# Kernel tuning notes

Hardware: AMD Instinct MI355X
Metric: run time of the kernel (lower is better)

The kernel has to match this reference:

```python
import jax, jax.numpy as jnp
import numpy as np

N, H, O, E, K = 131072, 128, 128, 8, 2


def setup_inputs() -> dict:
    key = jax.random.key(0)
    k1, k2, k3, k4 = jax.random.split(key, 4)
    x = jax.random.normal(k1, (N, H), dtype=jnp.float32)
    w_gate = jax.random.normal(k2, (H, E), dtype=jnp.float32) * 0.02
    w_noise = jax.random.normal(k3, (H, E), dtype=jnp.float32) * 0.02
    w_expert = jax.random.normal(k4, (E, H, O), dtype=jnp.float32) * (1.0 / np.sqrt(H))
    b_expert = jnp.zeros((E, O), dtype=jnp.float32)
    return {"x": x, "w_gate": w_gate, "w_noise": w_noise,
            "w_expert": w_expert, "b_expert": b_expert, "top_k": K}


def _gates(x, w_gate, top_k):
    # Noisy top-k gating (eval mode: noise term w_noise is inactive).
    logits = x @ w_gate                              # [N, E]
    top_vals, top_idx = jax.lax.top_k(logits, top_k)  # [N, K]
    top_gates = jax.nn.softmax(top_vals, axis=-1)     # renormalize over top-k
    n = logits.shape[0]
    rows = jnp.arange(n)[:, None]                     # [N, 1]
    gates = jnp.zeros_like(logits).at[rows, top_idx].set(top_gates)  # [N, E] sparse
    return gates


def reference(x, w_gate, w_noise, w_expert, b_expert, top_k):
    gates = _gates(x, w_gate, top_k)                                  # [N, E]
    # Dense (mathematically identical) dispatch/combine: every expert FFN
    # applied per token, weighted by its (mostly-zero) gate.
    expert_out = jnp.einsum('nh,eho->neo', x, w_expert) + b_expert     # [N, E, O]
    out = jnp.einsum('ne,neo->no', gates, expert_out)                  # [N, O]
    return out
```

## Files before the change

kernel.cpp:

```cpp
#include <hip/hip_runtime.h>
#include <math.h>

typedef __bf16 bf16x8 __attribute__((ext_vector_type(8)));
typedef float f32x16 __attribute__((ext_vector_type(16)));

#define NTOK 131072
#define HDIM 128
#define ODIM 128
#define NEXP 8

__device__ __forceinline__ unsigned short f2bf(float f){
  union { float f; unsigned u; } v; v.f = f;
  unsigned r = v.u + 0x7FFFu + ((v.u >> 16) & 1u);
  return (unsigned short)(r >> 16);
}

__global__ void pack_w(const float* __restrict__ we, const float* __restrict__ be,
                       unsigned short* __restrict__ pw){
  int f = blockIdx.x * 256 + threadIdx.x;
  int l  = f & 63;
  int kt = (f >> 6) % 9;
  int emt = f / (64 * 9);
  int mt = emt & 3;
  int e  = emt >> 2;
  int o  = (mt << 5) + (l & 31);
  unsigned short vals[8];
#pragma unroll
  for (int j = 0; j < 8; ++j){
    int kl = ((l >> 5) << 3) + j;
    float v;
    if (kt < 8){
      int h = kt * 16 + kl;
      v = we[(e * HDIM + h) * ODIM + o];
    } else {
      v = (kl == 0) ? be[e * ODIM + o] : 0.0f;
    }
    vals[j] = f2bf(v);
  }
  *(bf16x8*)(pw + (size_t)f * 8) = *(bf16x8*)vals;
}

__launch_bounds__(256, 3)
__global__ void moe_fused(const float* __restrict__ x, const float* __restrict__ wg,
                          const unsigned short* __restrict__ pw, float* __restrict__ out){
  __shared__ char lds[33792 + 4096 + 2048];
  float* xs            = (float*)lds;
  unsigned short* frag = (unsigned short*)lds;
  float* tb            = (float*)lds;
  float* wgt           = (float*)(lds + 33792);
  float* glds          = (float*)(lds + 33792 + 4096);

  int t = threadIdx.x;
  size_t tokbase = (size_t)blockIdx.x * 64;

  {
    float4 v = ((const float4*)wg)[t];
    int h = t >> 1, e0 = (t & 1) * 4;
    wgt[(e0 + 0) * 128 + h] = v.x;
    wgt[(e0 + 1) * 128 + h] = v.y;
    wgt[(e0 + 2) * 128 + h] = v.z;
    wgt[(e0 + 3) * 128 + h] = v.w;
  }
  {
    const float4* xsrc = (const float4*)(x + tokbase * HDIM);
#pragma unroll
    for (int i = 0; i < 8; ++i){
      int idx = i * 256 + t;
      int tok = idx >> 5, c = idx & 31;
      *(float4*)&xs[tok * 132 + c * 4] = xsrc[idx];
    }
  }
  __syncthreads();

  float4 cv[8];
#pragma unroll
  for (int i = 0; i < 8; ++i)
    cv[i] = *(float4*)&xs[(t >> 2) * 132 + (t & 3) * 32 + i * 4];

  {
    int tok = t & 63;
    const float* w0 = wgt + (t >> 6) * 2 * 128;
    const float* w1 = w0 + 128;
    float lg0 = 0.0f, lg1 = 0.0f;
#pragma unroll 8
    for (int c = 0; c < 32; ++c){
      float4 v = *(float4*)&xs[tok * 132 + c * 4];
      lg0 += v.x * w0[c * 4] + v.y * w0[c * 4 + 1] + v.z * w0[c * 4 + 2] + v.w * w0[c * 4 + 3];
      lg1 += v.x * w1[c * 4] + v.y * w1[c * 4 + 1] + v.z * w1[c * 4 + 2] + v.w * w1[c * 4 + 3];
    }
    int e0 = (t >> 6) * 2;
    glds[e0 * 64 + tok] = lg0;
    glds[(e0 + 1) * 64 + tok] = lg1;
  }
  __syncthreads();

  if (t < 64){
    float lg[8];
#pragma unroll
    for (int e = 0; e < 8; ++e) lg[e] = glds[e * 64 + t];
    int i1 = 0; float v1 = lg[0];
#pragma unroll
    for (int e = 1; e < 8; ++e) if (lg[e] > v1){ v1 = lg[e]; i1 = e; }
    int i2 = -1; float v2 = -3.4e38f;
#pragma unroll
    for (int e = 0; e < 8; ++e) if (e != i1 && lg[e] > v2){ v2 = lg[e]; i2 = e; }
    float ex = __expf(v2 - v1);
    float inv = 1.0f / (1.0f + ex);
#pragma unroll
    for (int e = 0; e < 8; ++e)
      glds[e * 64 + t] = (e == i1) ? inv : ((e == i2) ? ex * inv : 0.0f);
  }

  {
    int tokL = t >> 2, q = t & 3, tg = tokL >> 5;
#pragma unroll
    for (int jb = 0; jb < 4; ++jb){
      int h0 = q * 32 + jb * 8;
      int kt = h0 >> 4;
      int lslot = (tokL & 31) + 32 * ((h0 >> 3) & 1);
      float4 a = cv[2 * jb], b = cv[2 * jb + 1];
      unsigned long long lo = (unsigned long long)f2bf(a.x)
                            | ((unsigned long long)f2bf(a.y) << 16)
                            | ((unsigned long long)f2bf(a.z) << 32)
                            | ((unsigned long long)f2bf(a.w) << 48);
      unsigned long long hi = (unsigned long long)f2bf(b.x)
                            | ((unsigned long long)f2bf(b.y) << 16)
                            | ((unsigned long long)f2bf(b.z) << 32)
                            | ((unsigned long long)f2bf(b.w) << 48);
      unsigned long long* dst =
        (unsigned long long*)&frag[(((tg * 9) + kt) * 64 + lslot) * 8];
      dst[0] = lo; dst[1] = hi;
    }
    if (t < 128){
      int btg = t >> 6, bl = t & 63;
      unsigned long long* dst =
        (unsigned long long*)&frag[(((btg * 9) + 8) * 64 + bl) * 8];
      dst[0] = (bl < 32) ? 0x3F80ull : 0ull;
      dst[1] = 0ull;
    }
  }
  __syncthreads();

  int w = t >> 6, l = t & 63, l32 = l & 31, lh = l >> 5;

  f32x16 zero16;
#pragma unroll
  for (int i = 0; i < 16; ++i) zero16[i] = 0.0f;
  f32x16 tot0 = zero16, tot1 = zero16;

  const bf16x8* pwp = (const bf16x8*)pw;
#pragma unroll 1
  for (int e = 0; e < 8; ++e){
    float g0 = glds[e * 64 + l32];
    float g1 = glds[e * 64 + 32 + l32];
    const bf16x8* ap = pwp + ((size_t)(e * 4 + w) * 9) * 64 + l;
    f32x16 p0 = zero16, p1 = zero16;
#pragma unroll
    for (int kt = 0; kt < 9; ++kt){
      bf16x8 a  = ap[kt * 64];
      bf16x8 b0 = *(const bf16x8*)&frag[((0 * 9 + kt) * 64 + l) * 8];
      bf16x8 b1 = *(const bf16x8*)&frag[((1 * 9 + kt) * 64 + l) * 8];
      p0 = __builtin_amdgcn_mfma_f32_32x32x16_bf16(a, b0, p0, 0, 0, 0);
      p1 = __builtin_amdgcn_mfma_f32_32x32x16_bf16(a, b1, p1, 0, 0, 0);
    }
#pragma unroll
    for (int r = 0; r < 16; ++r){
      tot0[r] += g0 * p0[r];
      tot1[r] += g1 * p1[r];
    }
  }
  __syncthreads();

  {
#pragma unroll
    for (int rg = 0; rg < 4; ++rg){
      int o = w * 32 + rg * 8 + lh * 4;
      {
        int trow = 0 * 32 + l32;
        int cs = (o >> 2) ^ l32;
        *(float4*)&tb[trow * 128 + cs * 4] =
          make_float4(tot0[rg * 4 + 0], tot0[rg * 4 + 1], tot0[rg * 4 + 2], tot0[rg * 4 + 3]);
      }
      {
        int trow = 1 * 32 + l32;
        int cs = (o >> 2) ^ l32;
        *(float4*)&tb[trow * 128 + cs * 4] =
          make_float4(tot1[rg * 4 + 0], tot1[rg * 4 + 1], tot1[rg * 4 + 2], tot1[rg * 4 + 3]);
      }
    }
  }
  __syncthreads();
#pragma unroll
  for (int i = 0; i < 8; ++i){
    int idx = i * 256 + t;
    int trow = idx >> 5, c = idx & 31;
    int cs = c ^ (trow & 31);
    float4 v = *(float4*)&tb[trow * 128 + cs * 4];
    *(float4*)(out + (tokbase + trow) * ODIM + c * 4) = v;
  }
}

extern "C" void kernel_launch(void* const* d_in, const int* in_sizes, int n_in,
                              void* d_out, int out_size, void* d_ws, size_t ws_size,
                              hipStream_t stream){
  const float* x  = (const float*)d_in[0];
  const float* wg = (const float*)d_in[1];
  const float* we = (const float*)d_in[3];
  const float* be = (const float*)d_in[4];
  float* out = (float*)d_out;

  unsigned short* pw = (unsigned short*)d_ws;

  pack_w   <<<72,   256, 0, stream>>>(we, be, pw);
  moe_fused<<<2048, 256, 0, stream>>>(x, wg, pw, out);
}
```

Measured before the change: 152.8 us.

## Load x directly into registers, compute gating via shuffles, store output directly

Each thread now loads its own x slice straight from global memory into registers instead of staging the tile through LDS. Gating logits are computed per thread from global w_gate reads, reduced with lane shuffles, and top-2 is done redundantly by all four threads per token. The output transpose through LDS is dropped in favour of direct float4 global stores. This cuts LDS from about 40KB to about 20KB and removes several barriers, which should allow more resident blocks, at the cost of less coalesced x loads and output stores.

```diff
diff --git a/kernel.cpp b/kernel.cpp
--- a/kernel.cpp
+++ b/kernel.cpp
@@ -43,76 +43,65 @@
 __launch_bounds__(256, 3)
 __global__ void moe_fused(const float* __restrict__ x, const float* __restrict__ wg,
                           const unsigned short* __restrict__ pw, float* __restrict__ out){
-  __shared__ char lds[33792 + 4096 + 2048];
-  float* xs            = (float*)lds;
+  __shared__ char lds[18432 + 2048];
   unsigned short* frag = (unsigned short*)lds;
-  float* tb            = (float*)lds;
-  float* wgt           = (float*)(lds + 33792);
-  float* glds          = (float*)(lds + 33792 + 4096);
+  float* glds          = (float*)(lds + 18432);
 
   int t = threadIdx.x;
   size_t tokbase = (size_t)blockIdx.x * 64;
 
-  {
-    float4 v = ((const float4*)wg)[t];
-    int h = t >> 1, e0 = (t & 1) * 4;
-    wgt[(e0 + 0) * 128 + h] = v.x;
-    wgt[(e0 + 1) * 128 + h] = v.y;
-    wgt[(e0 + 2) * 128 + h] = v.z;
-    wgt[(e0 + 3) * 128 + h] = v.w;
+  int tokL = t >> 2, q = t & 3;
+  const float4* xr = (const float4*)(x + (tokbase + tokL) * HDIM + q * 32);
+  float4 cv[8];
+#pragma unroll
+  for (int i = 0; i < 8; ++i) cv[i] = xr[i];
+
+  float p[8];
+#pragma unroll
+  for (int e = 0; e < 8; ++e) p[e] = 0.0f;
+#pragma unroll
+  for (int i = 0; i < 8; ++i){
+    int hb = q * 32 + i * 4;
+    float4 w0a = *(const float4*)(wg + (hb + 0) * 8);
+    float4 w0b = *(const float4*)(wg + (hb + 0) * 8 + 4);
+    float4 w1a = *(const float4*)(wg + (hb + 1) * 8);
+    float4 w1b = *(const float4*)(wg + (hb + 1) * 8 + 4);
+    float4 w2a = *(const float4*)(wg + (hb + 2) * 8);
+    float4 w2b = *(const float4*)(wg + (hb + 2) * 8 + 4);
+    float4 w3a = *(const float4*)(wg + (hb + 3) * 8);
+    float4 w3b = *(const float4*)(wg + (hb + 3) * 8 + 4);
+    float4 v = cv[i];
+    p[0] += v.x * w0a.x + v.y * w1a.x + v.z * w2a.x + v.w * w3a.x;
+    p[1] += v.x * w0a.y + v.y * w1a.y + v.z * w2a.y + v.w * w3a.y;
+    p[2] += v.x * w0a.z + v.y * w1a.z + v.z * w2a.z + v.w * w3a.z;
+    p[3] += v.x * w0a.w + v.y * w1a.w + v.z * w2a.w + v.w * w3a.w;
+    p[4] += v.x * w0b.x + v.y * w1b.x + v.z * w2b.x + v.w * w3b.x;
+    p[5] += v.x * w0b.y + v.y * w1b.y + v.z * w2b.y + v.w * w3b.y;
+    p[6] += v.x * w0b.z + v.y * w1b.z + v.z * w2b.z + v.w * w3b.z;
+    p[7] += v.x * w0b.w + v.y * w1b.w + v.z * w2b.w + v.w * w3b.w;
+  }
+#pragma unroll
+  for (int e = 0; e < 8; ++e){
+    p[e] += __shfl_xor(p[e], 1);
+    p[e] += __shfl_xor(p[e], 2);
   }
   {
-    const float4* xsrc = (const float4*)(x + tokbase * HDIM);
+    int i1 = 0; float v1 = p[0];
 #pragma unroll
-    for (int i = 0; i < 8; ++i){
-      int idx = i * 256 + t;
-      int tok = idx >> 5, c = idx & 31;
-      *(float4*)&xs[tok * 132 + c * 4] = xsrc[idx];
-    }
-  }
-  __syncthreads();
-
-  float4 cv[8];
-#pragma unroll
-  for (int i = 0; i < 8; ++i)
-    cv[i] = *(float4*)&xs[(t >> 2) * 132 + (t & 3) * 32 + i * 4];
-
-  {
-    int tok = t & 63;
-    const float* w0 = wgt + (t >> 6) * 2 * 128;
-    const float* w1 = w0 + 128;
-    float lg0 = 0.0f, lg1 = 0.0f;
-#pragma unroll 8
-    for (int c = 0; c < 32; ++c){
-      float4 v = *(float4*)&xs[tok * 132 + c * 4];
-      lg0 += v.x * w0[c * 4] + v.y * w0[c * 4 + 1] + v.z * w0[c * 4 + 2] + v.w * w0[c * 4 + 3];
-      lg1 += v.x * w1[c * 4] + v.y * w1[c * 4 + 1] + v.z * w1[c * 4 + 2] + v.w * w1[c * 4 + 3];
-    }
-    int e0 = (t >> 6) * 2;
-    glds[e0 * 64 + tok] = lg0;
-    glds[(e0 + 1) * 64 + tok] = lg1;
-  }
-  __syncthreads();
-
-  if (t < 64){
-    float lg[8];
-#pragma unroll
-    for (int e = 0; e < 8; ++e) lg[e] = glds[e * 64 + t];
-    int i1 = 0; float v1 = lg[0];
-#pragma unroll
-    for (int e = 1; e < 8; ++e) if (lg[e] > v1){ v1 = lg[e]; i1 = e; }
+    for (int e = 1; e < 8; ++e) if (p[e] > v1){ v1 = p[e]; i1 = e; }
     int i2 = -1; float v2 = -3.4e38f;
 #pragma unroll
-    for (int e = 0; e < 8; ++e) if (e != i1 && lg[e] > v2){ v2 = lg[e]; i2 = e; }
+    for (int e = 0; e < 8; ++e) if (e != i1 && p[e] > v2){ v2 = p[e]; i2 = e; }
     float ex = __expf(v2 - v1);
     float inv = 1.0f / (1.0f + ex);
-#pragma unroll
-    for (int e = 0; e < 8; ++e)
-      glds[e * 64 + t] = (e == i1) ? inv : ((e == i2) ? ex * inv : 0.0f);
+    float gq  = (q     == i1) ? inv : ((q     == i2) ? ex * inv : 0.0f);
+    float gq4 = (q + 4 == i1) ? inv : ((q + 4 == i2) ? ex * inv : 0.0f);
+    glds[q * 64 + tokL]       = gq;
+    glds[(q + 4) * 64 + tokL] = gq4;
   }
 
   {
-    int tokL = t >> 2, q = t & 3, tg = tokL >> 5;
+    int tg = tokL >> 5;
 #pragma unroll
     for (int jb = 0; jb < 4; ++jb){
       int h0 = q * 32 + jb * 8;
@@ -169,34 +158,14 @@
       tot1[r] += g1 * p1[r];
     }
   }
-  __syncthreads();
 
-  {
 #pragma unroll
-    for (int rg = 0; rg < 4; ++rg){
-      int o = w * 32 + rg * 8 + lh * 4;
-      {
-        int trow = 0 * 32 + l32;
-        int cs = (o >> 2) ^ l32;
-        *(float4*)&tb[trow * 128 + cs * 4] =
-          make_float4(tot0[rg * 4 + 0], tot0[rg * 4 + 1], tot0[rg * 4 + 2], tot0[rg * 4 + 3]);
-      }
-      {
-        int trow = 1 * 32 + l32;
-        int cs = (o >> 2) ^ l32;
-        *(float4*)&tb[trow * 128 + cs * 4] =
-          make_float4(tot1[rg * 4 + 0], tot1[rg * 4 + 1], tot1[rg * 4 + 2], tot1[rg * 4 + 3]);
-      }
-    }
-  }
-  __syncthreads();
-#pragma unroll
-  for (int i = 0; i < 8; ++i){
-    int idx = i * 256 + t;
-    int trow = idx >> 5, c = idx & 31;
-    int cs = c ^ (trow & 31);
-    float4 v = *(float4*)&tb[trow * 128 + cs * 4];
-    *(float4*)(out + (tokbase + trow) * ODIM + c * 4) = v;
+  for (int rg = 0; rg < 4; ++rg){
+    int o = w * 32 + rg * 8 + lh * 4;
+    *(float4*)(out + (tokbase + l32) * ODIM + o) =
+      make_float4(tot0[rg * 4 + 0], tot0[rg * 4 + 1], tot0[rg * 4 + 2], tot0[rg * 4 + 3]);
+    *(float4*)(out + (tokbase + 32 + l32) * ODIM + o) =
+      make_float4(tot1[rg * 4 + 0], tot1[rg * 4 + 1], tot1[rg * 4 + 2], tot1[rg * 4 + 3]);
   }
 }
 
```

After: 199.1 us. 30.3% more time.
